# Kernel tuning notes

Measured on AMD Instinct MI355X. Metric: run time of the kernel, lower is better.

## Reference

```python
import jax, jax.numpy as jnp
import numpy as np

_LOG2PI = float(np.log(2.0 * np.pi))


def setup_inputs() -> dict:
    key = jax.random.key(0)
    ks = jax.random.split(key, 9)
    B, T, S, A, O = 64, 128, 512, 16, 4096
    regime = jax.random.randint(ks[0], (B,), 0, 2).astype(jnp.float32)
    obs = jax.random.randint(ks[1], (T + 1, B), 0, O, dtype=jnp.int32)
    rewards = jax.random.normal(ks[2], (T + 1, B), jnp.float32)
    dones = jnp.zeros((T + 1, B), jnp.float32)
    actions = jax.random.randint(ks[3], (T, B), 0, A, dtype=jnp.int32)
    prior_logits = jax.random.normal(ks[4], (S,), jnp.float32)
    trans_logits = jax.random.normal(ks[5], (A, S, S), jnp.float32)
    obs_logits = jax.random.normal(ks[6], (S, O), jnp.float32)
    policy_logits = jax.random.normal(ks[7], (S, A), jnp.float32)
    r_mu = jax.random.normal(ks[8], (S,), jnp.float32)
    r_logsig = jnp.zeros((S,), jnp.float32)
    return {"regime": regime, "obs": obs, "rewards": rewards, "dones": dones,
            "actions": actions, "prior_logits": prior_logits,
            "trans_logits": trans_logits, "obs_logits": obs_logits,
            "policy_logits": policy_logits, "r_mu": r_mu, "r_logsig": r_logsig}


def _log_prob(regime, obs, rewards, dones, actions, prior_logits, trans_logits,
              obs_logits, policy_logits, r_mu, r_logsig):
    # normalized log-prob tables (tabular instantiation of AugmentedModel)
    log_prior = jax.nn.log_softmax(prior_logits)              # [S]
    log_trans = jax.nn.log_softmax(trans_logits, axis=-1)     # [A,S,S]
    log_obs = jax.nn.log_softmax(obs_logits, axis=-1)         # [S,O]
    log_pol = jax.nn.log_softmax(policy_logits, axis=-1)      # [S,A]
    lse = jax.scipy.special.logsumexp

    def emis(o, r):  # log q(o|s) + log q(r|s) -> [B,S]
        lo = log_obs.T[o]                                      # [B,S] gather
        lr = (-0.5 * (((r[:, None] - r_mu[None, :]) * jnp.exp(-r_logsig)[None, :]) ** 2)
              - r_logsig[None, :] - 0.5 * _LOG2PI)             # [B,S]
        return lo + lr

    def act_term(a, done):  # masked log q(a|s) -> [B,S]
        la = log_pol.T[a]                                      # [B,S]
        la = jnp.where((done == 1.0)[:, None], jnp.zeros_like(la), la)
        la = jnp.where((regime == 1.0)[:, None], jnp.zeros_like(la), la)
        return la

    T = actions.shape[0]
    B = regime.shape[0]

    # t = 0
    was_done = jnp.zeros((B,), rewards.dtype)
    done0 = dones[0]
    lq_sorda = log_prior[None, :] + emis(obs[0], rewards[0]) + act_term(actions[0], done0)
    lq_orda = lse(lq_sorda, axis=-1) * (1.0 - was_done)        # [B]
    log_prob = lq_orda
    lq_s_h = lq_sorda - lq_orda[:, None]
    # belief propagation through transition: [B,S,1] + [B,S,S] -> lse over prev state
    lq_snext_h = lse(lq_s_h[:, :, None] + log_trans[actions[0]], axis=1)

    def step(carry, xs):  # t = 1 .. T-1 (has an action)
        log_prob, was_done, lq_s_hprev = carry
        o, r, d, a = xs
        done = jnp.maximum(was_done, d)
        lq = lq_s_hprev + emis(o, r) + act_term(a, done)
        lq_orda = lse(lq, axis=-1) * (1.0 - was_done)
        log_prob = jnp.where(jnp.isinf(log_prob), log_prob, log_prob + lq_orda)
        lq_s_h = lq - lq_orda[:, None]
        lq_snext = lse(lq_s_h[:, :, None] + log_trans[a], axis=1)
        return (log_prob, done, lq_snext), None

    xs = (obs[1:T], rewards[1:T], dones[1:T], actions[1:T])
    (log_prob, was_done, lq_s_hprev), _ = jax.lax.scan(
        step, (log_prob, done0, lq_snext_h), xs)

    # final step t = T (no action term)
    lq = lq_s_hprev + emis(obs[T], rewards[T])
    lq_ord = lse(lq, axis=-1) * (1.0 - was_done)
    log_prob = jnp.where(jnp.isinf(log_prob), log_prob, log_prob + lq_ord)
    return log_prob


def reference(regime, obs, rewards, dones, actions, prior_logits, trans_logits,
              obs_logits, policy_logits, r_mu, r_logsig):
    return _log_prob(regime, obs, rewards, dones, actions, prior_logits,
                     trans_logits, obs_logits, policy_logits, r_mu, r_logsig)
```

## Files before the change

### kernel.cpp

```cpp
#include <hip/hip_runtime.h>
#include <math.h>

#define DI __device__ __forceinline__

constexpr int BB = 64;
constexpr int TT = 128;
constexpr int SS = 512;
constexpr int AA = 16;
constexpr int OO = 4096;
constexpr float LOG2PI = 1.8378770664093453f;
constexpr float LOG4096 = 8.317766166719343f;

typedef float f32x4 __attribute__((ext_vector_type(4)));

DI void lds_barrier() {
    asm volatile("s_waitcnt lgkmcnt(0)\n\ts_barrier" ::: "memory");
}

DI unsigned int f32_to_e4m3(float x) {
    unsigned int u = __float_as_uint(x);
    unsigned int lsb = (u >> 20) & 1u;
    unsigned int rounded = u + 0x7ffffu + lsb;
    int e8 = (int)(rounded >> 23) - 120;
    unsigned int m3 = (rounded >> 20) & 7u;
    unsigned int norm = ((unsigned int)e8 << 3) | m3;
    int sub = __float2int_rn(x * 512.0f);
    return (e8 <= 0) ? (unsigned int)sub : norm;
}

DI float bflyMax(float v) {
#pragma unroll
    for (int off = 32; off; off >>= 1) v = fmaxf(v, __shfl_xor(v, off));
    return v;
}
DI float bflySum(float v) {
#pragma unroll
    for (int off = 32; off; off >>= 1) v += __shfl_xor(v, off);
    return v;
}
DI float halfMax(float v) {
#pragma unroll
    for (int off = 16; off; off >>= 1) v = fmaxf(v, __shfl_xor(v, off));
    return v;
}
DI float halfSum(float v) {
#pragma unroll
    for (int off = 16; off; off >>= 1) v += __shfl_xor(v, off);
    return v;
}

template <int NW>
DI float blockMax(float v, float* wr) {
    v = bflyMax(v);
    const int lane = threadIdx.x & 63, wv = threadIdx.x >> 6;
    if (lane == 0) wr[wv] = v;
    __syncthreads();
    float r = wr[0];
#pragma unroll
    for (int i = 1; i < NW; ++i) r = fmaxf(r, wr[i]);
    __syncthreads();
    return r;
}
template <int NW>
DI float blockSum(float v, float* wr) {
    v = bflySum(v);
    const int lane = threadIdx.x & 63, wv = threadIdx.x >> 6;
    if (lane == 0) wr[wv] = v;
    __syncthreads();
    float r = wr[0];
#pragma unroll
    for (int i = 1; i < NW; ++i) r += wr[i];
    __syncthreads();
    return r;
}


__global__ __launch_bounds__(1024) void k_pack(const float* __restrict__ tl,
                                               unsigned char* __restrict__ PB) {
    __shared__ unsigned char lds[16384];
    const int a = blockIdx.x >> 4;
    const int kt = blockIdx.x & 15;
    const int tid = threadIdx.x;
    const int r = tid >> 5;
    const int nt = tid & 31;
    const int k = kt * 32 + r;
    const float* row = tl + ((size_t)a * SS + k) * SS + nt * 16;

    float x[16];
#pragma unroll
    for (int i = 0; i < 4; ++i) {
        float4 v = ((const float4*)row)[i];
        x[4 * i] = v.x; x[4 * i + 1] = v.y; x[4 * i + 2] = v.z; x[4 * i + 3] = v.w;
    }
    float mx = -INFINITY;
#pragma unroll
    for (int i = 0; i < 16; ++i) mx = fmaxf(mx, x[i]);
    mx = halfMax(mx);
    float e[16];
    float sm = 0.f;
#pragma unroll
    for (int i = 0; i < 16; ++i) { e[i] = __expf(x[i] - mx); sm += e[i]; }
    sm = halfSum(sm);
    const float scale = 256.0f / sm;

    const int base = (nt >> 1) * 1024 + ((r >> 3) * 16) * 16 + (nt & 1) * 8 + (r & 7);
#pragma unroll
    for (int i = 0; i < 16; ++i) {
        lds[base + i * 16] = (unsigned char)f32_to_e4m3(e[i] * scale);
    }
    __syncthreads();

    ulonglong2* dst = (ulonglong2*)(PB + (size_t)(a * 16 + kt) * 16384);
    dst[tid] = ((const ulonglong2*)lds)[tid];
}

__global__ __launch_bounds__(256) void k_obs_stats(const float* __restrict__ ol,
                                                   float* __restrict__ mo,
                                                   float* __restrict__ lo) {
    __shared__ float wr[4];
    const int s = blockIdx.x;
    const float* in = ol + (size_t)s * OO;
    const int tid = threadIdx.x;
    float mx = -INFINITY;
    for (int i = tid; i < OO; i += 256) mx = fmaxf(mx, in[i]);
    float m = blockMax<4>(mx, wr);
    float sm = 0.f;
    for (int i = tid; i < OO; i += 256) sm += __expf(in[i] - m);
    float sum = blockSum<4>(sm, wr);
    if (tid == 0) { mo[s] = m; lo[s] = __logf(sum); }
}

__global__ __launch_bounds__(256) void k_obsT(const float* __restrict__ ol,
                                              const float* __restrict__ mo,
                                              const float* __restrict__ lo,
                                              float* __restrict__ obsT) {
    __shared__ float tile[64][65];
    const int tO = blockIdx.x % (OO / 64);
    const int tS = blockIdx.x / (OO / 64);
    const int o0 = tO * 64, s0 = tS * 64;
    const int cc = threadIdx.x & 63, rr = threadIdx.x >> 6;
#pragma unroll
    for (int j = 0; j < 16; ++j) {
        int r = rr + j * 4;
        tile[r][cc] = ol[(size_t)(s0 + r) * OO + o0 + cc] - mo[s0 + r] - lo[s0 + r];
    }
    __syncthreads();
#pragma unroll
    for (int j = 0; j < 16; ++j) {
        int r = rr + j * 4;
        obsT[(size_t)(o0 + r) * SS + s0 + cc] = tile[cc][r];
    }
}

__global__ __launch_bounds__(512) void k_main(
    const float* __restrict__ regime, const int* __restrict__ obs,
    const float* __restrict__ rewards, const float* __restrict__ dones,
    const int* __restrict__ actions, const float* __restrict__ prior_logits,
    const unsigned char* __restrict__ PB, const float* __restrict__ obsT,
    const float* __restrict__ policy_logits, const float* __restrict__ r_mu,
    const float* __restrict__ r_logsig, float* __restrict__ out) {
    __shared__ float wrm[8], wrs[8];
    __shared__ unsigned char p8[4 * 144 + 16];
    __shared__ float lqprev[SS];
    __shared__ int obs_l[TT + 1];
    __shared__ float rew_l[TT + 1];
    __shared__ float done_l[TT + 1];
    __shared__ int act_l[TT];

    const int b = blockIdx.x;
    const int tid = threadIdx.x;
    const int wv = tid >> 6, lane = tid & 63, quad = lane >> 4;
    const int s = tid;

    if (tid <= TT) {
        obs_l[tid] = obs[tid * BB + b];
        rew_l[tid] = rewards[tid * BB + b];
        done_l[tid] = dones[tid * BB + b];
        if (tid < TT) act_l[tid] = actions[tid * BB + b];
    }
    float la16[16];
    {
        const float4* pr4 = (const float4*)(policy_logits + (size_t)s * AA);
        float4 v0 = pr4[0], v1 = pr4[1], v2 = pr4[2], v3 = pr4[3];
        la16[0] = v0.x; la16[1] = v0.y; la16[2] = v0.z; la16[3] = v0.w;
        la16[4] = v1.x; la16[5] = v1.y; la16[6] = v1.z; la16[7] = v1.w;
        la16[8] = v2.x; la16[9] = v2.y; la16[10] = v2.z; la16[11] = v2.w;
        la16[12] = v3.x; la16[13] = v3.y; la16[14] = v3.z; la16[15] = v3.w;
        float mx = la16[0];
#pragma unroll
        for (int i = 1; i < 16; ++i) mx = fmaxf(mx, la16[i]);
        float sm = 0.f;
#pragma unroll
        for (int i = 0; i < 16; ++i) sm += __expf(la16[i] - mx);
        float ls = mx + __logf(sm);
#pragma unroll
        for (int i = 0; i < 16; ++i) la16[i] -= ls;
    }
    const float rm = r_mu[s];
    const float rls = r_logsig[s];
    const float inv_sig = __expf(-rls);
    const float reg = regime[b];

    float px = prior_logits[s];
    {
        float wm0 = bflyMax(px);
        if (lane == 0) wrm[wv] = wm0;
    }
    lds_barrier();
    float pm = wrm[0];
#pragma unroll
    for (int i = 1; i < 8; ++i) pm = fmaxf(pm, wrm[i]);
    {
        float ws0 = bflySum(__expf(px - pm));
        if (lane == 0) wrs[wv] = ws0;
    }
    lds_barrier();
    float psum = wrs[0];
#pragma unroll
    for (int i = 1; i < 8; ++i) psum += wrs[i];
    const float prior_reg = px - pm - __logf(psum);

    float obsv = obsT[(size_t)obs_l[0] * SS + s];

    float log_prob = 0.f;
    float was_done = 0.f;

    for (int t = 0; t < TT; ++t) {
        const float r = rew_l[t];
        const int a = __builtin_amdgcn_readfirstlane(act_l[t]);
        const float d = done_l[t];
        const float done = fmaxf(was_done, d);

        const unsigned char* Pw =
            PB + (size_t)a * (16 * 16384) + (size_t)(wv * 2048 + lane * 16);

        ulonglong2 fA[8], fB[8];
#pragma unroll
        for (int c = 0; c < 8; ++c) {
            fA[c] = *(const ulonglong2*)(Pw + c * 16384);
            fB[c] = *(const ulonglong2*)(Pw + c * 16384 + 1024);
        }
        float obsv_next = obsT[(size_t)obs_l[t + 1] * SS + s];
        asm volatile("" ::: "memory");

        float diff = (r - rm) * inv_sig;
        float emis = obsv - 0.5f * diff * diff - rls - 0.5f * LOG2PI;
        float base_in = (t == 0) ? prior_reg : lqprev[s];
        float la = la16[0];
#pragma unroll
        for (int i = 1; i < 16; ++i) la = (a == i) ? la16[i] : la;
        if (done == 1.0f || reg == 1.0f) la = 0.f;
        float lq = base_in + emis + la;

        float wmax = bflyMax(lq);
        if (lane == 0) wrm[wv] = wmax;
        lds_barrier();
        float m = wrm[0];
#pragma unroll
        for (int i = 1; i < 8; ++i) m = fmaxf(m, wrm[i]);

        float exv = __expf(lq - m);
        p8[((s >> 3) & 3) * 144 + (s >> 5) * 8 + (s & 7)] =
            (unsigned char)f32_to_e4m3(exv * 16.0f);
        float wsum = bflySum(exv);
        if (lane == 0) wrs[wv] = wsum;
        lds_barrier();
        float sum = wrs[0];
#pragma unroll
        for (int i = 1; i < 8; ++i) sum += wrs[i];
        float lse = m + __logf(sum);
        float lq_orda = lse * (1.0f - was_done);
        if (!isinf(log_prob)) log_prob += lq_orda;
        was_done = done;

        const float basev = m - lq_orda - LOG4096;
        f32x4 acc0 = {0.f, 0.f, 0.f, 0.f};
        f32x4 acc1 = {0.f, 0.f, 0.f, 0.f};
        f32x4 acc2 = {0.f, 0.f, 0.f, 0.f};
        f32x4 acc3 = {0.f, 0.f, 0.f, 0.f};

#define CHUNK(c)                                                                \
        {                                                                       \
            long af = *(const long long*)(p8 + quad * 144 + (c) * 8);           \
            acc0 = __builtin_amdgcn_mfma_f32_16x16x32_fp8_fp8((long)fA[(c) & 7].x, af, acc0, 0, 0, 0); \
            acc1 = __builtin_amdgcn_mfma_f32_16x16x32_fp8_fp8((long)fA[(c) & 7].y, af, acc1, 0, 0, 0); \
            acc2 = __builtin_amdgcn_mfma_f32_16x16x32_fp8_fp8((long)fB[(c) & 7].x, af, acc2, 0, 0, 0); \
            acc3 = __builtin_amdgcn_mfma_f32_16x16x32_fp8_fp8((long)fB[(c) & 7].y, af, acc3, 0, 0, 0); \
            if ((c) + 8 < 16) {                                                 \
                fA[(c) & 7] = *(const ulonglong2*)(Pw + ((c) + 8) * 16384);     \
                fB[(c) & 7] = *(const ulonglong2*)(Pw + ((c) + 8) * 16384 + 1024); \
            }                                                                   \
        }
        CHUNK(0)  CHUNK(1)  CHUNK(2)  CHUNK(3)
        CHUNK(4)  CHUNK(5)  CHUNK(6)  CHUNK(7)
        CHUNK(8)  CHUNK(9)  CHUNK(10) CHUNK(11)
        CHUNK(12) CHUNK(13) CHUNK(14) CHUNK(15)
#undef CHUNK

        if (lane < 16) {
            lqprev[wv * 64 + lane]      = basev + __logf(acc0[0]);
            lqprev[wv * 64 + 16 + lane] = basev + __logf(acc1[0]);
            lqprev[wv * 64 + 32 + lane] = basev + __logf(acc2[0]);
            lqprev[wv * 64 + 48 + lane] = basev + __logf(acc3[0]);
        }
        asm volatile("s_waitcnt lgkmcnt(0)" ::: "memory");
        obsv = obsv_next;
    }

    {
        const float r = rew_l[TT];
        float diff = (r - rm) * inv_sig;
        float emis = obsv - 0.5f * diff * diff - rls - 0.5f * LOG2PI;
        float lq = lqprev[s] + emis;
        float wmax = bflyMax(lq);
        if (lane == 0) wrm[wv] = wmax;
        lds_barrier();
        float m = wrm[0];
#pragma unroll
        for (int i = 1; i < 8; ++i) m = fmaxf(m, wrm[i]);
        float wsum = bflySum(__expf(lq - m));
        if (lane == 0) wrs[wv] = wsum;
        lds_barrier();
        float sum = wrs[0];
#pragma unroll
        for (int i = 1; i < 8; ++i) sum += wrs[i];
        float lse = m + __logf(sum);
        float lq_ord = lse * (1.0f - was_done);
        if (!isinf(log_prob)) log_prob += lq_ord;
    }

    if (tid == 0) out[b] = log_prob;
}

extern "C" void kernel_launch(void* const* d_in, const int* in_sizes, int n_in,
                              void* d_out, int out_size, void* d_ws, size_t ws_size,
                              hipStream_t stream) {
    const float* regime = (const float*)d_in[0];
    const int* obs = (const int*)d_in[1];
    const float* rewards = (const float*)d_in[2];
    const float* dones = (const float*)d_in[3];
    const int* actions = (const int*)d_in[4];
    const float* prior_logits = (const float*)d_in[5];
    const float* trans_logits = (const float*)d_in[6];
    const float* obs_logits = (const float*)d_in[7];
    const float* policy_logits = (const float*)d_in[8];
    const float* r_mu = (const float*)d_in[9];
    const float* r_logsig = (const float*)d_in[10];
    float* out = (float*)d_out;

    char* ws = (char*)d_ws;
    unsigned char* PB = (unsigned char*)ws;
    float* obsT = (float*)(ws + (size_t)AA * SS * SS);
    float* mo = (float*)(ws + (size_t)AA * SS * SS + (size_t)OO * SS * 4);
    float* lo = mo + SS;

    k_pack<<<256, 1024, 0, stream>>>(trans_logits, PB);
    k_obs_stats<<<SS, 256, 0, stream>>>(obs_logits, mo, lo);
    k_obsT<<<(OO / 64) * (SS / 64), 256, 0, stream>>>(obs_logits, mo, lo, obsT);
    k_main<<<BB, 512, 0, stream>>>(regime, obs, rewards, dones, actions, prior_logits,
                                   PB, obsT, policy_logits, r_mu, r_logsig, out);
}
```

Before: 492.7 us.

## Prefetch next step's transition fragments across time steps and keep state in registers

Double-buffers the fp8 transition-matrix fragments in registers, so the second half of each step's MFMA chain issues the loads for the next step's action slice. This hides global load latency at the start of each time step. It also drops the shared-memory lqprev round trip and redistributes MFMA results to lanes with cross-lane shuffles. The launch bound is raised to request two blocks per CU. The extra fragment registers (four buffers) may push register pressure or force spills under the tighter occupancy bound.

After: 476.8 us. 1.03x faster.

```diff
diff --git a/kernel.cpp b/kernel.cpp
--- a/kernel.cpp
+++ b/kernel.cpp
@@ -152,7 +152,7 @@
     }
 }
 
-__global__ __launch_bounds__(512) void k_main(
+__global__ __launch_bounds__(512, 2) void k_main(
     const float* __restrict__ regime, const int* __restrict__ obs,
     const float* __restrict__ rewards, const float* __restrict__ dones,
     const int* __restrict__ actions, const float* __restrict__ prior_logits,
@@ -161,7 +161,6 @@
     const float* __restrict__ r_logsig, float* __restrict__ out) {
     __shared__ float wrm[8], wrs[8];
     __shared__ unsigned char p8[4 * 144 + 16];
-    __shared__ float lqprev[SS];
     __shared__ int obs_l[TT + 1];
     __shared__ float rew_l[TT + 1];
     __shared__ float done_l[TT + 1];
@@ -171,6 +170,8 @@
     const int tid = threadIdx.x;
     const int wv = tid >> 6, lane = tid & 63, quad = lane >> 4;
     const int s = tid;
+    const int wvl16 = wv * 2048 + lane * 16;
+    const int p8idx = ((s >> 3) & 3) * 144 + (s >> 5) * 8 + (s & 7);
 
     if (tid <= TT) {
         obs_l[tid] = obs[tid * BB + b];
@@ -218,100 +219,119 @@
     float psum = wrs[0];
 #pragma unroll
     for (int i = 1; i < 8; ++i) psum += wrs[i];
-    const float prior_reg = px - pm - __logf(psum);
-
+    float base_reg = px - pm - __logf(psum);
+
+    ulonglong2 fA[8], fB[8], gA[8], gB[8];
+    {
+        const int a0 = __builtin_amdgcn_readfirstlane(act_l[0]);
+        const unsigned char* P0 = PB + (size_t)a0 * (16 * 16384) + wvl16;
+#pragma unroll
+        for (int c = 0; c < 8; ++c) {
+            fA[c] = *(const ulonglong2*)(P0 + c * 16384);
+            fB[c] = *(const ulonglong2*)(P0 + c * 16384 + 1024);
+        }
+    }
     float obsv = obsT[(size_t)obs_l[0] * SS + s];
 
     float log_prob = 0.f;
     float was_done = 0.f;
 
-    for (int t = 0; t < TT; ++t) {
-        const float r = rew_l[t];
-        const int a = __builtin_amdgcn_readfirstlane(act_l[t]);
-        const float d = done_l[t];
-        const float done = fmaxf(was_done, d);
-
-        const unsigned char* Pw =
-            PB + (size_t)a * (16 * 16384) + (size_t)(wv * 2048 + lane * 16);
-
-        ulonglong2 fA[8], fB[8];
-#pragma unroll
-        for (int c = 0; c < 8; ++c) {
-            fA[c] = *(const ulonglong2*)(Pw + c * 16384);
-            fB[c] = *(const ulonglong2*)(Pw + c * 16384 + 1024);
-        }
-        float obsv_next = obsT[(size_t)obs_l[t + 1] * SS + s];
-        asm volatile("" ::: "memory");
-
-        float diff = (r - rm) * inv_sig;
-        float emis = obsv - 0.5f * diff * diff - rls - 0.5f * LOG2PI;
-        float base_in = (t == 0) ? prior_reg : lqprev[s];
-        float la = la16[0];
-#pragma unroll
-        for (int i = 1; i < 16; ++i) la = (a == i) ? la16[i] : la;
-        if (done == 1.0f || reg == 1.0f) la = 0.f;
-        float lq = base_in + emis + la;
-
-        float wmax = bflyMax(lq);
-        if (lane == 0) wrm[wv] = wmax;
-        lds_barrier();
-        float m = wrm[0];
-#pragma unroll
-        for (int i = 1; i < 8; ++i) m = fmaxf(m, wrm[i]);
-
-        float exv = __expf(lq - m);
-        p8[((s >> 3) & 3) * 144 + (s >> 5) * 8 + (s & 7)] =
-            (unsigned char)f32_to_e4m3(exv * 16.0f);
-        float wsum = bflySum(exv);
-        if (lane == 0) wrs[wv] = wsum;
-        lds_barrier();
-        float sum = wrs[0];
-#pragma unroll
-        for (int i = 1; i < 8; ++i) sum += wrs[i];
-        float lse = m + __logf(sum);
-        float lq_orda = lse * (1.0f - was_done);
-        if (!isinf(log_prob)) log_prob += lq_orda;
-        was_done = done;
-
-        const float basev = m - lq_orda - LOG4096;
-        f32x4 acc0 = {0.f, 0.f, 0.f, 0.f};
-        f32x4 acc1 = {0.f, 0.f, 0.f, 0.f};
-        f32x4 acc2 = {0.f, 0.f, 0.f, 0.f};
-        f32x4 acc3 = {0.f, 0.f, 0.f, 0.f};
-
-#define CHUNK(c)                                                                \
-        {                                                                       \
-            long af = *(const long long*)(p8 + quad * 144 + (c) * 8);           \
-            acc0 = __builtin_amdgcn_mfma_f32_16x16x32_fp8_fp8((long)fA[(c) & 7].x, af, acc0, 0, 0, 0); \
-            acc1 = __builtin_amdgcn_mfma_f32_16x16x32_fp8_fp8((long)fA[(c) & 7].y, af, acc1, 0, 0, 0); \
-            acc2 = __builtin_amdgcn_mfma_f32_16x16x32_fp8_fp8((long)fB[(c) & 7].x, af, acc2, 0, 0, 0); \
-            acc3 = __builtin_amdgcn_mfma_f32_16x16x32_fp8_fp8((long)fB[(c) & 7].y, af, acc3, 0, 0, 0); \
-            if ((c) + 8 < 16) {                                                 \
-                fA[(c) & 7] = *(const ulonglong2*)(Pw + ((c) + 8) * 16384);     \
-                fB[(c) & 7] = *(const ulonglong2*)(Pw + ((c) + 8) * 16384 + 1024); \
-            }                                                                   \
-        }
-        CHUNK(0)  CHUNK(1)  CHUNK(2)  CHUNK(3)
-        CHUNK(4)  CHUNK(5)  CHUNK(6)  CHUNK(7)
-        CHUNK(8)  CHUNK(9)  CHUNK(10) CHUNK(11)
-        CHUNK(12) CHUNK(13) CHUNK(14) CHUNK(15)
-#undef CHUNK
-
-        if (lane < 16) {
-            lqprev[wv * 64 + lane]      = basev + __logf(acc0[0]);
-            lqprev[wv * 64 + 16 + lane] = basev + __logf(acc1[0]);
-            lqprev[wv * 64 + 32 + lane] = basev + __logf(acc2[0]);
-            lqprev[wv * 64 + 48 + lane] = basev + __logf(acc3[0]);
-        }
-        asm volatile("s_waitcnt lgkmcnt(0)" ::: "memory");
-        obsv = obsv_next;
-    }
+#define CHUNK_L(c, CA, CB)                                                      \
+    {                                                                           \
+        long af = *(const long long*)(p8 + quad * 144 + (c) * 8);               \
+        acc0 = __builtin_amdgcn_mfma_f32_16x16x32_fp8_fp8((long)CA[(c)].x, af, acc0, 0, 0, 0); \
+        acc1 = __builtin_amdgcn_mfma_f32_16x16x32_fp8_fp8((long)CA[(c)].y, af, acc1, 0, 0, 0); \
+        acc2 = __builtin_amdgcn_mfma_f32_16x16x32_fp8_fp8((long)CB[(c)].x, af, acc2, 0, 0, 0); \
+        acc3 = __builtin_amdgcn_mfma_f32_16x16x32_fp8_fp8((long)CB[(c)].y, af, acc3, 0, 0, 0); \
+        CA[(c)] = *(const ulonglong2*)(Pw_ + ((c) + 8) * 16384);                \
+        CB[(c)] = *(const ulonglong2*)(Pw_ + ((c) + 8) * 16384 + 1024);         \
+    }
+#define CHUNK_H(c, CA, CB, NA, NB)                                              \
+    {                                                                           \
+        long af = *(const long long*)(p8 + quad * 144 + (c) * 8);               \
+        acc0 = __builtin_amdgcn_mfma_f32_16x16x32_fp8_fp8((long)CA[(c) - 8].x, af, acc0, 0, 0, 0); \
+        acc1 = __builtin_amdgcn_mfma_f32_16x16x32_fp8_fp8((long)CA[(c) - 8].y, af, acc1, 0, 0, 0); \
+        acc2 = __builtin_amdgcn_mfma_f32_16x16x32_fp8_fp8((long)CB[(c) - 8].x, af, acc2, 0, 0, 0); \
+        acc3 = __builtin_amdgcn_mfma_f32_16x16x32_fp8_fp8((long)CB[(c) - 8].y, af, acc3, 0, 0, 0); \
+        NA[(c) - 8] = *(const ulonglong2*)(Pn_ + ((c) - 8) * 16384);            \
+        NB[(c) - 8] = *(const ulonglong2*)(Pn_ + ((c) - 8) * 16384 + 1024);     \
+    }
+
+#define STEP(T, CA, CB, NA, NB)                                                 \
+    {                                                                           \
+        const int t_ = (T);                                                     \
+        const float r_ = rew_l[t_];                                             \
+        const int a_ = __builtin_amdgcn_readfirstlane(act_l[t_]);               \
+        const float d_ = done_l[t_];                                            \
+        const float done_ = fmaxf(was_done, d_);                                \
+        const unsigned char* Pw_ = PB + (size_t)a_ * (16 * 16384) + wvl16;      \
+        const int tn_ = (t_ + 1 < TT) ? t_ + 1 : 0;                             \
+        const int an_ = __builtin_amdgcn_readfirstlane(act_l[tn_]);             \
+        const unsigned char* Pn_ = PB + (size_t)an_ * (16 * 16384) + wvl16;     \
+        float obsv_next_ = obsT[(size_t)obs_l[t_ + 1] * SS + s];                \
+                \
+        float diff_ = (r_ - rm) * inv_sig;                                      \
+        float emis_ = obsv - 0.5f * diff_ * diff_ - rls - 0.5f * LOG2PI;        \
+        float la_ = la16[0];                                                    \
+        _Pragma("unroll")                                                       \
+        for (int i = 1; i < 16; ++i) la_ = (a_ == i) ? la16[i] : la_;           \
+        if (done_ == 1.0f || reg == 1.0f) la_ = 0.f;                            \
+        float lq_ = base_reg + emis_ + la_;                                     \
+        float wmax_ = bflyMax(lq_);                                             \
+        if (lane == 0) wrm[wv] = wmax_;                                         \
+        lds_barrier();                                                  \
+        float m_ = wrm[0];                                                      \
+        _Pragma("unroll")                                                       \
+        for (int i = 1; i < 8; ++i) m_ = fmaxf(m_, wrm[i]);                     \
+        float exv_ = __expf(lq_ - m_);                                          \
+        p8[p8idx] = (unsigned char)f32_to_e4m3(exv_ * 16.0f);                   \
+        float wsum_ = bflySum(exv_);                                            \
+        if (lane == 0) wrs[wv] = wsum_;                                         \
+        lds_barrier();                                   \
+        float sum_ = wrs[0];                                                    \
+        _Pragma("unroll")                                                       \
+        for (int i = 1; i < 8; ++i) sum_ += wrs[i];                             \
+        float lse_ = m_ + __logf(sum_);                                         \
+        float lqo_ = lse_ * (1.0f - was_done);                                  \
+        if (!isinf(log_prob)) log_prob += lqo_;                                 \
+        was_done = done_;                                                       \
+        \
+        const float basev_ = m_ - lqo_ - LOG4096;                               \
+        f32x4 acc0 = {0.f, 0.f, 0.f, 0.f};                                      \
+        f32x4 acc1 = {0.f, 0.f, 0.f, 0.f};                                      \
+        f32x4 acc2 = {0.f, 0.f, 0.f, 0.f};                                      \
+        f32x4 acc3 = {0.f, 0.f, 0.f, 0.f};                                      \
+        CHUNK_L(0, CA, CB)  CHUNK_L(1, CA, CB)  CHUNK_L(2, CA, CB)              \
+        CHUNK_L(3, CA, CB)  CHUNK_L(4, CA, CB)  CHUNK_L(5, CA, CB)              \
+        CHUNK_L(6, CA, CB)  CHUNK_L(7, CA, CB)                                  \
+        CHUNK_H(8, CA, CB, NA, NB)   CHUNK_H(9, CA, CB, NA, NB)                 \
+        CHUNK_H(10, CA, CB, NA, NB)  CHUNK_H(11, CA, CB, NA, NB)                \
+        CHUNK_H(12, CA, CB, NA, NB)  CHUNK_H(13, CA, CB, NA, NB)                \
+        CHUNK_H(14, CA, CB, NA, NB)  CHUNK_H(15, CA, CB, NA, NB)                \
+           \
+        float t0_ = __shfl(acc0[0], lane & 15);                                 \
+        float t1_ = __shfl(acc1[0], lane & 15);                                 \
+        float t2_ = __shfl(acc2[0], lane & 15);                                 \
+        float t3_ = __shfl(acc3[0], lane & 15);                                 \
+        float av_ = quad == 0 ? t0_ : (quad == 1 ? t1_ : (quad == 2 ? t2_ : t3_)); \
+        base_reg = basev_ + __logf(av_);                                        \
+        obsv = obsv_next_;                                                      \
+        asm volatile("" ::: "memory");      \
+    }
+
+    for (int t = 0; t < TT; t += 2) {
+        STEP(t, fA, fB, gA, gB)
+        STEP(t + 1, gA, gB, fA, fB)
+    }
+#undef STEP
+#undef CHUNK_L
+#undef CHUNK_H
 
     {
         const float r = rew_l[TT];
         float diff = (r - rm) * inv_sig;
         float emis = obsv - 0.5f * diff * diff - rls - 0.5f * LOG2PI;
-        float lq = lqprev[s] + emis;
+        float lq = base_reg + emis;
         float wmax = bflyMax(lq);
         if (lane == 0) wrm[wv] = wmax;
         lds_barrier();
```

## Prefetch all transition fragments upfront and keep next-state log-probs in registers

Applied to the files above, without the earlier changes.

The per-step fragment loads now fetch all 16 chunks of the transition tile into registers at the top of the step, replacing the double-buffered reload inside the MFMA loop, and a sched_barrier pins that ordering. The next-state log-probabilities are moved between lanes with shuffles and kept in a register, so the shared lqprev array and its store/wait round-trip are gone. Launch bounds request two blocks per CU. The aim is to hide global-load latency and drop an LDS round-trip from the serial time loop. The cost is much higher register pressure from 32 ulonglong2 fragments, which could cause spills or conflict with the two-block occupancy target.

New measurement: 513.9 us. 1.04x slower.

```diff
diff --git a/kernel.cpp b/kernel.cpp
--- a/kernel.cpp
+++ b/kernel.cpp
@@ -152,7 +152,7 @@
     }
 }
 
-__global__ __launch_bounds__(512) void k_main(
+__global__ __launch_bounds__(512, 2) void k_main(
     const float* __restrict__ regime, const int* __restrict__ obs,
     const float* __restrict__ rewards, const float* __restrict__ dones,
     const int* __restrict__ actions, const float* __restrict__ prior_logits,
@@ -160,8 +160,7 @@
     const float* __restrict__ policy_logits, const float* __restrict__ r_mu,
     const float* __restrict__ r_logsig, float* __restrict__ out) {
     __shared__ float wrm[8], wrs[8];
-    __shared__ unsigned char p8[4 * 144 + 16];
-    __shared__ float lqprev[SS];
+    __shared__ alignas(16) unsigned char p8[4 * 144 + 16];
     __shared__ int obs_l[TT + 1];
     __shared__ float rew_l[TT + 1];
     __shared__ float done_l[TT + 1];
@@ -171,6 +170,8 @@
     const int tid = threadIdx.x;
     const int wv = tid >> 6, lane = tid & 63, quad = lane >> 4;
     const int s = tid;
+    const int wvl16 = wv * 2048 + lane * 16;
+    const int p8idx = ((s >> 3) & 3) * 144 + (s >> 5) * 8 + (s & 7);
 
     if (tid <= TT) {
         obs_l[tid] = obs[tid * BB + b];
@@ -218,7 +219,7 @@
     float psum = wrs[0];
 #pragma unroll
     for (int i = 1; i < 8; ++i) psum += wrs[i];
-    const float prior_reg = px - pm - __logf(psum);
+    float base_reg = px - pm - __logf(psum);
 
     float obsv = obsT[(size_t)obs_l[0] * SS + s];
 
@@ -230,27 +231,24 @@
         const int a = __builtin_amdgcn_readfirstlane(act_l[t]);
         const float d = done_l[t];
         const float done = fmaxf(was_done, d);
-
-        const unsigned char* Pw =
-            PB + (size_t)a * (16 * 16384) + (size_t)(wv * 2048 + lane * 16);
-
-        ulonglong2 fA[8], fB[8];
-#pragma unroll
-        for (int c = 0; c < 8; ++c) {
-            fA[c] = *(const ulonglong2*)(Pw + c * 16384);
-            fB[c] = *(const ulonglong2*)(Pw + c * 16384 + 1024);
+        const unsigned char* Pw = PB + (size_t)a * (16 * 16384) + wvl16;
+
+        ulonglong2 fA[16], fB[16];
+#pragma unroll
+        for (int c = 0; c < 16; ++c) {
+            fA[c] = *(const ulonglong2*)(Pw + (size_t)c * 16384);
+            fB[c] = *(const ulonglong2*)(Pw + (size_t)c * 16384 + 1024);
         }
         float obsv_next = obsT[(size_t)obs_l[t + 1] * SS + s];
-        asm volatile("" ::: "memory");
+        __builtin_amdgcn_sched_barrier(0);
 
         float diff = (r - rm) * inv_sig;
         float emis = obsv - 0.5f * diff * diff - rls - 0.5f * LOG2PI;
-        float base_in = (t == 0) ? prior_reg : lqprev[s];
         float la = la16[0];
 #pragma unroll
         for (int i = 1; i < 16; ++i) la = (a == i) ? la16[i] : la;
         if (done == 1.0f || reg == 1.0f) la = 0.f;
-        float lq = base_in + emis + la;
+        float lq = base_reg + emis + la;
 
         float wmax = bflyMax(lq);
         if (lane == 0) wrm[wv] = wmax;
@@ -260,8 +258,7 @@
         for (int i = 1; i < 8; ++i) m = fmaxf(m, wrm[i]);
 
         float exv = __expf(lq - m);
-        p8[((s >> 3) & 3) * 144 + (s >> 5) * 8 + (s & 7)] =
-            (unsigned char)f32_to_e4m3(exv * 16.0f);
+        p8[p8idx] = (unsigned char)f32_to_e4m3(exv * 16.0f);
         float wsum = bflySum(exv);
         if (lane == 0) wrs[wv] = wsum;
         lds_barrier();
@@ -282,14 +279,10 @@
 #define CHUNK(c)                                                                \
         {                                                                       \
             long af = *(const long long*)(p8 + quad * 144 + (c) * 8);           \
-            acc0 = __builtin_amdgcn_mfma_f32_16x16x32_fp8_fp8((long)fA[(c) & 7].x, af, acc0, 0, 0, 0); \
-            acc1 = __builtin_amdgcn_mfma_f32_16x16x32_fp8_fp8((long)fA[(c) & 7].y, af, acc1, 0, 0, 0); \
-            acc2 = __builtin_amdgcn_mfma_f32_16x16x32_fp8_fp8((long)fB[(c) & 7].x, af, acc2, 0, 0, 0); \
-            acc3 = __builtin_amdgcn_mfma_f32_16x16x32_fp8_fp8((long)fB[(c) & 7].y, af, acc3, 0, 0, 0); \
-            if ((c) + 8 < 16) {                                                 \
-                fA[(c) & 7] = *(const ulonglong2*)(Pw + ((c) + 8) * 16384);     \
-                fB[(c) & 7] = *(const ulonglong2*)(Pw + ((c) + 8) * 16384 + 1024); \
-            }                                                                   \
+            acc0 = __builtin_amdgcn_mfma_f32_16x16x32_fp8_fp8((long)fA[(c)].x, af, acc0, 0, 0, 0); \
+            acc1 = __builtin_amdgcn_mfma_f32_16x16x32_fp8_fp8((long)fA[(c)].y, af, acc1, 0, 0, 0); \
+            acc2 = __builtin_amdgcn_mfma_f32_16x16x32_fp8_fp8((long)fB[(c)].x, af, acc2, 0, 0, 0); \
+            acc3 = __builtin_amdgcn_mfma_f32_16x16x32_fp8_fp8((long)fB[(c)].y, af, acc3, 0, 0, 0); \
         }
         CHUNK(0)  CHUNK(1)  CHUNK(2)  CHUNK(3)
         CHUNK(4)  CHUNK(5)  CHUNK(6)  CHUNK(7)
@@ -297,13 +290,12 @@
         CHUNK(12) CHUNK(13) CHUNK(14) CHUNK(15)
 #undef CHUNK
 
-        if (lane < 16) {
-            lqprev[wv * 64 + lane]      = basev + __logf(acc0[0]);
-            lqprev[wv * 64 + 16 + lane] = basev + __logf(acc1[0]);
-            lqprev[wv * 64 + 32 + lane] = basev + __logf(acc2[0]);
-            lqprev[wv * 64 + 48 + lane] = basev + __logf(acc3[0]);
-        }
-        asm volatile("s_waitcnt lgkmcnt(0)" ::: "memory");
+        float t0 = __shfl(acc0[0], lane & 15);
+        float t1 = __shfl(acc1[0], lane & 15);
+        float t2 = __shfl(acc2[0], lane & 15);
+        float t3 = __shfl(acc3[0], lane & 15);
+        float av = quad == 0 ? t0 : (quad == 1 ? t1 : (quad == 2 ? t2 : t3));
+        base_reg = basev + __logf(av);
         obsv = obsv_next;
     }
 
@@ -311,7 +303,7 @@
         const float r = rew_l[TT];
         float diff = (r - rm) * inv_sig;
         float emis = obsv - 0.5f * diff * diff - rls - 0.5f * LOG2PI;
-        float lq = lqprev[s] + emis;
+        float lq = base_reg + emis;
         float wmax = bflyMax(lq);
         if (lane == 0) wrm[wv] = wmax;
         lds_barrier();
```
